# Optimization experiments

Hardware: AMD Instinct MI355X
Metric: run time of the kernel (lower is better)

## Reference

```python
import jax, jax.numpy as jnp
import numpy as np

B, C, G, E, R, T, L, K = 8, 192, 256, 384, 4, 8192, 3, 3
DILATIONS = (1, 3, 9)
EPS = 1e-5


def setup_inputs() -> dict:
    key = jax.random.key(0)
    ks = jax.random.split(key, 16)
    s = 0.05
    return {
        'x': jax.random.normal(ks[0], (B, C, T), jnp.float32),
        'x_mask': jnp.ones((B, 1, T), jnp.float32),
        'g': jax.random.normal(ks[1], (B, G, 1), jnp.float32),
        'dconv_w': jax.random.normal(ks[2], (L, C, K), jnp.float32) * s,
        'dconv_b': jax.random.normal(ks[3], (L, C), jnp.float32) * s,
        'ln_gamma': jnp.ones((L, C), jnp.float32),
        'ln_beta': jnp.zeros((L, C), jnp.float32),
        'p1_w': jax.random.normal(ks[4], (L, E, C), jnp.float32) * s,
        'p1_b': jax.random.normal(ks[5], (L, E), jnp.float32) * s,
        'p1_ain_w': jax.random.normal(ks[6], (L, C * R, G), jnp.float32) * 0.01,
        'p1_ain_b': jnp.zeros((L, C * R), jnp.float32),
        'p1_aout_w': jax.random.normal(ks[7], (L, E * R, G), jnp.float32) * 0.01,
        'p1_aout_b': jnp.zeros((L, E * R), jnp.float32),
        'p2_w': jax.random.normal(ks[8], (L, C, E), jnp.float32) * s,
        'p2_b': jax.random.normal(ks[9], (L, C), jnp.float32) * s,
        'p2_ain_w': jax.random.normal(ks[10], (L, E * R, G), jnp.float32) * 0.01,
        'p2_ain_b': jnp.zeros((L, E * R), jnp.float32),
        'p2_aout_w': jax.random.normal(ks[11], (L, C * R, G), jnp.float32) * 0.01,
        'p2_aout_b': jnp.zeros((L, C * R), jnp.float32),
    }


def _causal_dconv(x, w, b, dilation):
    # x: [B,C,T]; w: [C,K] depthwise kernel; matches flip/pad/conv/flip in torch module
    xf = jnp.flip(x, 2)
    xf = jnp.pad(xf, ((0, 0), (0, 0), (0, (K - 1) * dilation)))
    y = jax.lax.conv_general_dilated(
        xf, w[:, None, :], window_strides=(1,), padding='VALID',
        rhs_dilation=(dilation,), dimension_numbers=('NCH', 'OIH', 'NCH'),
        feature_group_count=C)
    y = y + b[None, :, None]
    return jnp.flip(y, 2)


def _layernorm_c(x, gamma, beta):
    # LayerNorm over channel axis (axis=1)
    mu = jnp.mean(x, axis=1, keepdims=True)
    var = jnp.mean(jnp.square(x - mu), axis=1, keepdims=True)
    xn = (x - mu) * jax.lax.rsqrt(var + EPS)
    return xn * gamma[None, :, None] + beta[None, :, None]


def _lora(x, g2, w_main, b_main, ain_w, ain_b, aout_w, aout_b, cin, cout):
    # main 1x1 conv
    x_ = jnp.einsum('oc,bcl->bol', w_main, x) + b_main[None, :, None]
    a_in = (g2 @ ain_w.T + ain_b).reshape(-1, cin, R)      # [B,cin,R]
    a_out = (g2 @ aout_w.T + aout_b).reshape(-1, R, cout)  # [B,R,cout]
    t = jnp.einsum('bcl,bcr->brl', x, a_in)
    low = jnp.einsum('brl,brc->bcl', t, a_out)
    return x_ + low


def reference(x, x_mask, g, dconv_w, dconv_b, ln_gamma, ln_beta,
              p1_w, p1_b, p1_ain_w, p1_ain_b, p1_aout_w, p1_aout_b,
              p2_w, p2_b, p2_ain_w, p2_ain_b, p2_aout_w, p2_aout_b):
    g2 = g[:, :, 0]  # [B,G]
    x = x * x_mask
    for i in range(L):
        residual = x
        h = _causal_dconv(x, dconv_w[i], dconv_b[i], DILATIONS[i])
        h = _layernorm_c(h, ln_gamma[i], ln_beta[i])
        h = h * x_mask
        h = _lora(h, g2, p1_w[i], p1_b[i], p1_ain_w[i], p1_ain_b[i],
                  p1_aout_w[i], p1_aout_b[i], C, E)
        h = jax.nn.gelu(h, approximate=False)
        h = _lora(h, g2, p2_w[i], p2_b[i], p2_ain_w[i], p2_ain_b[i],
                  p2_aout_w[i], p2_aout_b[i], E, C)
        x = residual + h
    return x
```

## Files before the change

kernel.cpp:

```cpp
#include <hip/hip_runtime.h>
#include <hip/hip_bf16.h>

#define B_ 8
#define C_ 192
#define G_ 256
#define E_ 384
#define R_ 4
#define T_ 8192
#define L_ 3
#define K_ 3

typedef __attribute__((ext_vector_type(4))) float f32x4;
typedef __attribute__((ext_vector_type(8))) short bf16x8;
typedef __attribute__((ext_vector_type(4))) short bf16x4;

static __device__ __forceinline__ float bf2f(short u) {
    union { float f; unsigned int i; } z;
    z.i = ((unsigned int)(unsigned short)u) << 16;
    return z.f;
}

static __device__ __forceinline__ float gelu_fast(float x) {
    float x2 = x * x;
    float inner = fmaf(0.044715f * x, x2, x);
    float e = __expf(1.5957691216057308f * inner);
    float r = 1.0f / (e + 1.0f);
    float t = fmaf(-2.0f, r, 1.0f);
    float s = 0.5f * x;
    return fmaf(s, t, s);
}

__global__ __launch_bounds__(256) void adapters_kernel(
    const float* __restrict__ g2,
    const float* __restrict__ w0, const float* __restrict__ bi0, float* __restrict__ o0,
    const float* __restrict__ w1, const float* __restrict__ bi1, float* __restrict__ o1,
    const float* __restrict__ w2, const float* __restrict__ bi2, float* __restrict__ o2,
    const float* __restrict__ w3, const float* __restrict__ bi3, float* __restrict__ o3)
{
    const int N0 = L_ * B_ * (C_ * R_);
    const int N1 = L_ * B_ * (E_ * R_);
    int idx = blockIdx.x * 256 + threadIdx.x;
    const float* w; const float* bi; float* o; int rows; int li;
    if (idx < N0)                      { w=w0; bi=bi0; o=o0; rows=C_*R_; li=idx; }
    else if ((idx -= N0) < N1)         { w=w1; bi=bi1; o=o1; rows=E_*R_; li=idx; }
    else if ((idx -= N1) < N1)         { w=w2; bi=bi2; o=o2; rows=E_*R_; li=idx; }
    else if ((idx -= N1) < N0)         { w=w3; bi=bi3; o=o3; rows=C_*R_; li=idx; }
    else return;
    int bb = li & 7;
    int lr = li >> 3;
    const float4* wr = (const float4*)(w + (size_t)lr * G_);
    const float4* gb = (const float4*)(g2 + (size_t)bb * G_);
    float s = bi[lr];
#pragma unroll 8
    for (int g = 0; g < G_ / 4; ++g) {
        float4 a = gb[g], b = wr[g];
        s = fmaf(a.x, b.x, s); s = fmaf(a.y, b.y, s);
        s = fmaf(a.z, b.z, s); s = fmaf(a.w, b.w, s);
    }
    o[((size_t)(lr / rows) * B_ + bb) * rows + (lr % rows)] = s;
}

__global__ __launch_bounds__(256) void builds_kernel(
    const float* __restrict__ p1w, const float* __restrict__ p2w,
    const float* __restrict__ A1in, const float* __restrict__ A1out,
    const float* __restrict__ A2in, const float* __restrict__ A2out,
    __hip_bfloat16* __restrict__ W1, __hip_bfloat16* __restrict__ W2)
{
    const int W1B = (L_ * B_ * E_ * C_) / 256;
    int blk = blockIdx.x;
    if (blk < W1B) {
        int idx = blk * 256 + threadIdx.x;
        int c = idx % C_;
        int e = (idx / C_) % E_;
        int b = (idx / (C_ * E_)) % B_;
        int l = idx / (C_ * E_ * B_);
        float v = p1w[((size_t)l * E_ + e) * C_ + c];
        const float* ai = A1in + ((size_t)l * B_ + b) * (C_ * R_);
        const float* ao = A1out + ((size_t)l * B_ + b) * (R_ * E_);
#pragma unroll
        for (int r = 0; r < R_; ++r) v = fmaf(ai[c * R_ + r], ao[r * E_ + e], v);
        W1[idx] = __float2bfloat16(v);
    } else {
        int idx = (blk - W1B) * 256 + threadIdx.x;
        int e = idx % E_;
        int c = (idx / E_) % C_;
        int b = (idx / (C_ * E_)) % B_;
        int l = idx / (C_ * E_ * B_);
        float v = p2w[((size_t)l * C_ + c) * E_ + e];
        const float* ai = A2in + ((size_t)l * B_ + b) * (E_ * R_);
        const float* ao = A2out + ((size_t)l * B_ + b) * (R_ * C_);
#pragma unroll
        for (int r = 0; r < R_; ++r) v = fmaf(ai[e * R_ + r], ao[r * C_ + c], v);
        W2[idx] = __float2bfloat16(v);
    }
}

__global__ __launch_bounds__(256) void transpose_in_kernel(
    const float* __restrict__ x, const float* __restrict__ mask,
    __hip_bfloat16* __restrict__ xw)
{
    __shared__ float tile[64][65];
    int b = blockIdx.z, c0 = blockIdx.y * 64, t0 = blockIdx.x * 64;
#pragma unroll
    for (int it = 0; it < 4; ++it) {
        int i = it * 256 + threadIdx.x;
        int r = i >> 4, cq = i & 15;
        float4 xv = *(const float4*)(&x[((size_t)b * C_ + c0 + r) * T_ + t0 + cq * 4]);
        float4 mv = *(const float4*)(&mask[(size_t)b * T_ + t0 + cq * 4]);
        tile[r][cq * 4 + 0] = xv.x * mv.x;
        tile[r][cq * 4 + 1] = xv.y * mv.y;
        tile[r][cq * 4 + 2] = xv.z * mv.z;
        tile[r][cq * 4 + 3] = xv.w * mv.w;
    }
    __syncthreads();
#pragma unroll
    for (int it = 0; it < 4; ++it) {
        int i = it * 256 + threadIdx.x;
        int r = i >> 4, cq = i & 15;
        union { __hip_bfloat16 h[4]; int2 i2; } u;
#pragma unroll
        for (int j = 0; j < 4; ++j) u.h[j] = __float2bfloat16(tile[cq * 4 + j][r]);
        *(int2*)(&xw[((size_t)b * T_ + t0 + r) * C_ + c0 + cq * 4]) = u.i2;
    }
}

__global__ __launch_bounds__(256, 2) void ffn_fused_kernel(
    const __hip_bfloat16* __restrict__ xin, __hip_bfloat16* __restrict__ xout,
    const float* __restrict__ dw, const float* __restrict__ db,
    const float* __restrict__ gamma, const float* __restrict__ beta,
    const float* __restrict__ mask,
    const __hip_bfloat16* __restrict__ W1, const float* __restrict__ b1,
    const __hip_bfloat16* __restrict__ W2, const float* __restrict__ b2,
    int dil, float* __restrict__ outF)
{
    __shared__ __align__(16) char smem[75776];
    __hip_bfloat16 (*Hs)[C_ + 8]  = (__hip_bfloat16 (*)[C_ + 8])smem;
    __hip_bfloat16 (*H1s)[E_ + 8] = (__hip_bfloat16 (*)[E_ + 8])(smem + 25600);
    float (*Tile)[68] = (float (*)[68])smem;

    const int bid = blockIdx.x;
    const int b = bid & 7;
    const int t0 = (bid >> 3) * 64;
    const int tid = threadIdx.x;
    const int wv = tid >> 6, lane = tid & 63;
    const int llo = lane & 15, lhi = lane >> 4;
    const size_t xbase = (size_t)b * T_ * C_;

    {
        const int grp = tid >> 4, gl = tid & 15;
        const int cbase = gl * 12;
        float4 wf[9], dbf[3], gaf[3], bef[3];
#pragma unroll
        for (int q = 0; q < 9; ++q) wf[q] = *(const float4*)(dw + cbase * 3 + q * 4);
#pragma unroll
        for (int q = 0; q < 3; ++q) {
            dbf[q] = *(const float4*)(db + cbase + q * 4);
            gaf[q] = *(const float4*)(gamma + cbase + q * 4);
            bef[q] = *(const float4*)(beta + cbase + q * 4);
        }
#pragma unroll
        for (int rr = 0; rr < 4; ++rr) {
            int tl = grp * 4 + rr;
            int t = t0 + tl;
            float v[12];
#pragma unroll
            for (int j = 0; j < 12; ++j) v[j] = ((const float*)dbf)[j];
#pragma unroll
            for (int k3 = 0; k3 < 3; ++k3) {
                int tt = t - k3 * dil;
                if (tt >= 0) {
                    const __hip_bfloat16* rp = xin + xbase + (size_t)tt * C_ + cbase;
#pragma unroll
                    for (int q = 0; q < 3; ++q) {
                        bf16x4 xv = *(const bf16x4*)(rp + q * 4);
#pragma unroll
                        for (int jj = 0; jj < 4; ++jj) {
                            int j = q * 4 + jj;
                            v[j] = fmaf(((const float*)wf)[j * 3 + k3], bf2f(xv[jj]), v[j]);
                        }
                    }
                }
            }
            float s = 0.f, sq = 0.f;
#pragma unroll
            for (int j = 0; j < 12; ++j) { s += v[j]; sq = fmaf(v[j], v[j], sq); }
#pragma unroll
            for (int o = 1; o <= 8; o <<= 1) {
                s += __shfl_xor(s, o, 64);
                sq += __shfl_xor(sq, o, 64);
            }
            float mu = s * (1.f / C_);
            float var = fmaf(sq, 1.f / C_, -mu * mu);
            float rs = rsqrtf(var + 1e-5f);
            float m = mask[(size_t)b * T_ + t];
            union { __hip_bfloat16 h[12]; int2 i2[3]; } u;
#pragma unroll
            for (int j = 0; j < 12; ++j) {
                float xn = (v[j] - mu) * rs;
                u.h[j] = __float2bfloat16(
                    fmaf(xn, ((const float*)gaf)[j], ((const float*)bef)[j]) * m);
            }
#pragma unroll
            for (int q = 0; q < 3; ++q)
                *(int2*)(&Hs[tl][cbase + q * 4]) = u.i2[q];
        }
    }
    __syncthreads();

    const __hip_bfloat16* w1p = W1 + (size_t)b * E_ * C_
        + (size_t)(wv * 96 + llo) * C_ + lhi * 8;
    f32x4 acc1[6][4] = {};
    {
        bf16x8 af[3][6], bfr[2][4];
#pragma unroll
        for (int mf = 0; mf < 6; ++mf) {
            af[0][mf] = *(const bf16x8*)(w1p + (size_t)mf * 16 * C_);
            af[1][mf] = *(const bf16x8*)(w1p + (size_t)mf * 16 * C_ + 32);
        }
#pragma unroll
        for (int nf = 0; nf < 4; ++nf)
            bfr[0][nf] = *(const bf16x8*)(&Hs[nf * 16 + llo][lhi * 8]);
#pragma unroll
        for (int kc = 0; kc < 6; ++kc) {
            const int cur = kc % 3;
            const int pf  = (kc + 2) % 3;
            const int bc  = kc & 1;
            if (kc < 4) {
#pragma unroll
                for (int mf = 0; mf < 6; ++mf)
                    af[pf][mf] = *(const bf16x8*)(w1p + (size_t)mf * 16 * C_ + (kc + 2) * 32);
            }
            if (kc < 5) {
#pragma unroll
                for (int nf = 0; nf < 4; ++nf)
                    bfr[bc ^ 1][nf] = *(const bf16x8*)(&Hs[nf * 16 + llo][(kc + 1) * 32 + lhi * 8]);
            }
#pragma unroll
            for (int mf = 0; mf < 6; ++mf)
#pragma unroll
                for (int nf = 0; nf < 4; ++nf)
                    acc1[mf][nf] = __builtin_amdgcn_mfma_f32_16x16x32_bf16(
                        af[cur][mf], bfr[bc][nf], acc1[mf][nf], 0, 0, 0);
        }
    }

#pragma unroll
    for (int mf = 0; mf < 6; ++mf) {
        int e0 = wv * 96 + mf * 16 + lhi * 4;
        float4 b1v = *(const float4*)(b1 + e0);
#pragma unroll
        for (int nf = 0; nf < 4; ++nf) {
            union { __hip_bfloat16 h[4]; int2 i2; } u;
#pragma unroll
            for (int j = 0; j < 4; ++j) {
                float xx = acc1[mf][nf][j] + ((const float*)&b1v)[j];
                u.h[j] = __float2bfloat16(gelu_fast(xx));
            }
            *(int2*)(&H1s[nf * 16 + llo][e0]) = u.i2;
        }
    }
    __syncthreads();

    const __hip_bfloat16* w2p = W2 + (size_t)b * C_ * E_
        + (size_t)(wv * 48 + llo) * E_ + lhi * 8;
    f32x4 acc2[3][4] = {};
    {
        bf16x8 af[3][3], bfr[2][4];
#pragma unroll
        for (int mf = 0; mf < 3; ++mf) {
            af[0][mf] = *(const bf16x8*)(w2p + (size_t)mf * 16 * E_);
            af[1][mf] = *(const bf16x8*)(w2p + (size_t)mf * 16 * E_ + 32);
        }
#pragma unroll
        for (int nf = 0; nf < 4; ++nf)
            bfr[0][nf] = *(const bf16x8*)(&H1s[nf * 16 + llo][lhi * 8]);
#pragma unroll
        for (int kc = 0; kc < 12; ++kc) {
            const int cur = kc % 3;
            const int pf  = (kc + 2) % 3;
            const int bc  = kc & 1;
            if (kc < 10) {
#pragma unroll
                for (int mf = 0; mf < 3; ++mf)
                    af[pf][mf] = *(const bf16x8*)(w2p + (size_t)mf * 16 * E_ + (kc + 2) * 32);
            }
            if (kc < 11) {
#pragma unroll
                for (int nf = 0; nf < 4; ++nf)
                    bfr[bc ^ 1][nf] = *(const bf16x8*)(&H1s[nf * 16 + llo][(kc + 1) * 32 + lhi * 8]);
            }
#pragma unroll
            for (int mf = 0; mf < 3; ++mf)
#pragma unroll
                for (int nf = 0; nf < 4; ++nf)
                    acc2[mf][nf] = __builtin_amdgcn_mfma_f32_16x16x32_bf16(
                        af[cur][mf], bfr[bc][nf], acc2[mf][nf], 0, 0, 0);
        }
    }

    if (outF == nullptr) {
#pragma unroll
        for (int mf = 0; mf < 3; ++mf) {
            int c0 = wv * 48 + mf * 16 + lhi * 4;
            float4 b2v = *(const float4*)(b2 + c0);
#pragma unroll
            for (int nf = 0; nf < 4; ++nf) {
                int t = t0 + nf * 16 + llo;
                const __hip_bfloat16* pr = xin + xbase + (size_t)t * C_ + c0;
                __hip_bfloat16* po = xout + xbase + (size_t)t * C_ + c0;
                union { __hip_bfloat16 h[4]; int2 i2; } ui, uo;
                ui.i2 = *(const int2*)pr;
#pragma unroll
                for (int j = 0; j < 4; ++j)
                    uo.h[j] = __float2bfloat16(
                        bf2f(*(short*)&ui.h[j]) + acc2[mf][nf][j] + ((const float*)&b2v)[j]);
                *(int2*)po = uo.i2;
            }
        }
    } else {
        __syncthreads();
#pragma unroll
        for (int mf = 0; mf < 3; ++mf) {
            int c0 = wv * 48 + mf * 16 + lhi * 4;
            float4 b2v = *(const float4*)(b2 + c0);
#pragma unroll
            for (int nf = 0; nf < 4; ++nf) {
                int tl = nf * 16 + llo;
                const __hip_bfloat16* pr = xin + xbase + (size_t)(t0 + tl) * C_ + c0;
                union { __hip_bfloat16 h[4]; int2 i2; } ui;
                ui.i2 = *(const int2*)pr;
#pragma unroll
                for (int j = 0; j < 4; ++j)
                    Tile[c0 + j][tl] =
                        bf2f(*(short*)&ui.h[j]) + acc2[mf][nf][j] + ((const float*)&b2v)[j];
            }
        }
        __syncthreads();
#pragma unroll
        for (int it = 0; it < 12; ++it) {
            int i = it * 256 + tid;
            int r = i >> 4, tq = i & 15;
            float4 o = *(const float4*)(&Tile[r][tq * 4]);
            *(float4*)(&outF[((size_t)b * C_ + r) * T_ + t0 + tq * 4]) = o;
        }
    }
}

extern "C" void kernel_launch(void* const* d_in, const int* in_sizes, int n_in,
                              void* d_out, int out_size, void* d_ws, size_t ws_size,
                              hipStream_t stream) {
    const float* x        = (const float*)d_in[0];
    const float* x_mask   = (const float*)d_in[1];
    const float* g        = (const float*)d_in[2];
    const float* dconv_w  = (const float*)d_in[3];
    const float* dconv_b  = (const float*)d_in[4];
    const float* ln_gamma = (const float*)d_in[5];
    const float* ln_beta  = (const float*)d_in[6];
    const float* p1_w     = (const float*)d_in[7];
    const float* p1_b     = (const float*)d_in[8];
    const float* p1_ain_w = (const float*)d_in[9];
    const float* p1_ain_b = (const float*)d_in[10];
    const float* p1_aout_w= (const float*)d_in[11];
    const float* p1_aout_b= (const float*)d_in[12];
    const float* p2_w     = (const float*)d_in[13];
    const float* p2_b     = (const float*)d_in[14];
    const float* p2_ain_w = (const float*)d_in[15];
    const float* p2_ain_b = (const float*)d_in[16];
    const float* p2_aout_w= (const float*)d_in[17];
    const float* p2_aout_b= (const float*)d_in[18];

    char* ws = (char*)d_ws;
    size_t off = 0;
    __hip_bfloat16* xwA = (__hip_bfloat16*)(ws + off); off += (size_t)B_ * T_ * C_ * 2;
    __hip_bfloat16* xwB = (__hip_bfloat16*)(ws + off); off += (size_t)B_ * T_ * C_ * 2;
    __hip_bfloat16* W1 = (__hip_bfloat16*)(ws + off);  off += (size_t)L_ * B_ * E_ * C_ * 2;
    __hip_bfloat16* W2 = (__hip_bfloat16*)(ws + off);  off += (size_t)L_ * B_ * C_ * E_ * 2;
    float* A1in  = (float*)(ws + off); off += (size_t)L_ * B_ * C_ * R_ * 4;
    float* A1out = (float*)(ws + off); off += (size_t)L_ * B_ * R_ * E_ * 4;
    float* A2in  = (float*)(ws + off); off += (size_t)L_ * B_ * E_ * R_ * 4;
    float* A2out = (float*)(ws + off); off += (size_t)L_ * B_ * R_ * C_ * 4;

    {
        int total = L_ * B_ * (2 * C_ * R_ + 2 * E_ * R_);
        adapters_kernel<<<(total + 255) / 256, 256, 0, stream>>>(
            g,
            p1_ain_w, p1_ain_b, A1in,
            p1_aout_w, p1_aout_b, A1out,
            p2_ain_w, p2_ain_b, A2in,
            p2_aout_w, p2_aout_b, A2out);
    }
    {
        int w1blocks = (L_ * B_ * E_ * C_) / 256;
        builds_kernel<<<2 * w1blocks, 256, 0, stream>>>(
            p1_w, p2_w, A1in, A1out, A2in, A2out, W1, W2);
    }

    transpose_in_kernel<<<dim3(T_ / 64, C_ / 64, B_), 256, 0, stream>>>(x, x_mask, xwA);

    const int DILS[3] = {1, 3, 9};
    __hip_bfloat16* bufs[2] = {xwA, xwB};
    for (int l = 0; l < L_; ++l) {
        float* outF = (l == L_ - 1) ? (float*)d_out : nullptr;
        ffn_fused_kernel<<<(T_ / 64) * B_, 256, 0, stream>>>(
            bufs[l & 1], bufs[(l & 1) ^ 1],
            dconv_w + l * C_ * K_, dconv_b + l * C_,
            ln_gamma + l * C_, ln_beta + l * C_, x_mask,
            W1 + (size_t)l * B_ * E_ * C_, p1_b + l * E_,
            W2 + (size_t)l * B_ * C_ * E_, p2_b + l * C_, DILS[l], outF);
    }
}
```

Before: 231.8 us.

## Give each wave its own 16-token slice and drop block-wide barriers

Work is now split by token instead of by output channel: each wave takes 16 tokens and computes all 384 hidden and 192 output channels for them, keeping its activations in a private shared-memory slice. This removes the two __syncthreads between the conv/layernorm, first GEMM and second GEMM stages. In exchange, every wave reads the full W1 and W2 from global or L2 memory with no register double-buffering, which is 4x more weight traffic per block. It also holds 24 accumulator fragments per lane, which raises register pressure.

```diff
diff --git a/kernel.cpp b/kernel.cpp
--- a/kernel.cpp
+++ b/kernel.cpp
@@ -134,20 +134,22 @@
     int dil, float* __restrict__ outF)
 {
     __shared__ __align__(16) char smem[75776];
-    __hip_bfloat16 (*Hs)[C_ + 8]  = (__hip_bfloat16 (*)[C_ + 8])smem;
-    __hip_bfloat16 (*H1s)[E_ + 8] = (__hip_bfloat16 (*)[E_ + 8])(smem + 25600);
-    float (*Tile)[68] = (float (*)[68])smem;
-
     const int bid = blockIdx.x;
     const int b = bid & 7;
     const int t0 = (bid >> 3) * 64;
     const int tid = threadIdx.x;
     const int wv = tid >> 6, lane = tid & 63;
     const int llo = lane & 15, lhi = lane >> 4;
+    const int t0w = t0 + wv * 16;
     const size_t xbase = (size_t)b * T_ * C_;
 
+    __hip_bfloat16 (*Hw)[C_ + 8] =
+        (__hip_bfloat16 (*)[C_ + 8])(smem + (size_t)wv * 16 * (C_ + 8) * 2);
+    __hip_bfloat16 (*H1w)[E_ + 8] =
+        (__hip_bfloat16 (*)[E_ + 8])(smem + 25600 + (size_t)wv * 16 * (E_ + 8) * 2);
+
     {
-        const int grp = tid >> 4, gl = tid & 15;
+        const int grp = lane >> 4, gl = lane & 15;
         const int cbase = gl * 12;
         float4 wf[9], dbf[3], gaf[3], bef[3];
 #pragma unroll
@@ -161,7 +163,7 @@
 #pragma unroll
         for (int rr = 0; rr < 4; ++rr) {
             int tl = grp * 4 + rr;
-            int t = t0 + tl;
+            int t = t0w + tl;
             float v[12];
 #pragma unroll
             for (int j = 0; j < 12; ++j) v[j] = ((const float*)dbf)[j];
@@ -202,137 +204,79 @@
             }
 #pragma unroll
             for (int q = 0; q < 3; ++q)
-                *(int2*)(&Hs[tl][cbase + q * 4]) = u.i2[q];
-        }
-    }
-    __syncthreads();
-
-    const __hip_bfloat16* w1p = W1 + (size_t)b * E_ * C_
-        + (size_t)(wv * 96 + llo) * C_ + lhi * 8;
-    f32x4 acc1[6][4] = {};
-    {
-        bf16x8 af[3][6], bfr[2][4];
-#pragma unroll
-        for (int mf = 0; mf < 6; ++mf) {
-            af[0][mf] = *(const bf16x8*)(w1p + (size_t)mf * 16 * C_);
-            af[1][mf] = *(const bf16x8*)(w1p + (size_t)mf * 16 * C_ + 32);
-        }
-#pragma unroll
-        for (int nf = 0; nf < 4; ++nf)
-            bfr[0][nf] = *(const bf16x8*)(&Hs[nf * 16 + llo][lhi * 8]);
-#pragma unroll
-        for (int kc = 0; kc < 6; ++kc) {
-            const int cur = kc % 3;
-            const int pf  = (kc + 2) % 3;
-            const int bc  = kc & 1;
-            if (kc < 4) {
-#pragma unroll
-                for (int mf = 0; mf < 6; ++mf)
-                    af[pf][mf] = *(const bf16x8*)(w1p + (size_t)mf * 16 * C_ + (kc + 2) * 32);
-            }
-            if (kc < 5) {
-#pragma unroll
-                for (int nf = 0; nf < 4; ++nf)
-                    bfr[bc ^ 1][nf] = *(const bf16x8*)(&Hs[nf * 16 + llo][(kc + 1) * 32 + lhi * 8]);
-            }
-#pragma unroll
-            for (int mf = 0; mf < 6; ++mf)
-#pragma unroll
-                for (int nf = 0; nf < 4; ++nf)
-                    acc1[mf][nf] = __builtin_amdgcn_mfma_f32_16x16x32_bf16(
-                        af[cur][mf], bfr[bc][nf], acc1[mf][nf], 0, 0, 0);
-        }
-    }
-
-#pragma unroll
-    for (int mf = 0; mf < 6; ++mf) {
-        int e0 = wv * 96 + mf * 16 + lhi * 4;
+                *(int2*)(&Hw[tl][cbase + q * 4]) = u.i2[q];
+        }
+    }
+
+    const __hip_bfloat16* w1p = W1 + (size_t)b * E_ * C_ + (size_t)llo * C_ + lhi * 8;
+    f32x4 acc1[24] = {};
+#pragma unroll
+    for (int kc = 0; kc < 6; ++kc) {
+        bf16x8 bfr = *(const bf16x8*)(&Hw[llo][kc * 32 + lhi * 8]);
+#pragma unroll
+        for (int mf = 0; mf < 24; ++mf) {
+            bf16x8 af = *(const bf16x8*)(w1p + (size_t)mf * 16 * C_ + kc * 32);
+            acc1[mf] = __builtin_amdgcn_mfma_f32_16x16x32_bf16(af, bfr, acc1[mf], 0, 0, 0);
+        }
+    }
+
+#pragma unroll
+    for (int mf = 0; mf < 24; ++mf) {
+        int e0 = mf * 16 + lhi * 4;
         float4 b1v = *(const float4*)(b1 + e0);
-#pragma unroll
-        for (int nf = 0; nf < 4; ++nf) {
-            union { __hip_bfloat16 h[4]; int2 i2; } u;
-#pragma unroll
-            for (int j = 0; j < 4; ++j) {
-                float xx = acc1[mf][nf][j] + ((const float*)&b1v)[j];
-                u.h[j] = __float2bfloat16(gelu_fast(xx));
-            }
-            *(int2*)(&H1s[nf * 16 + llo][e0]) = u.i2;
-        }
-    }
-    __syncthreads();
-
-    const __hip_bfloat16* w2p = W2 + (size_t)b * C_ * E_
-        + (size_t)(wv * 48 + llo) * E_ + lhi * 8;
-    f32x4 acc2[3][4] = {};
-    {
-        bf16x8 af[3][3], bfr[2][4];
-#pragma unroll
-        for (int mf = 0; mf < 3; ++mf) {
-            af[0][mf] = *(const bf16x8*)(w2p + (size_t)mf * 16 * E_);
-            af[1][mf] = *(const bf16x8*)(w2p + (size_t)mf * 16 * E_ + 32);
-        }
-#pragma unroll
-        for (int nf = 0; nf < 4; ++nf)
-            bfr[0][nf] = *(const bf16x8*)(&H1s[nf * 16 + llo][lhi * 8]);
-#pragma unroll
-        for (int kc = 0; kc < 12; ++kc) {
-            const int cur = kc % 3;
-            const int pf  = (kc + 2) % 3;
-            const int bc  = kc & 1;
-            if (kc < 10) {
-#pragma unroll
-                for (int mf = 0; mf < 3; ++mf)
-                    af[pf][mf] = *(const bf16x8*)(w2p + (size_t)mf * 16 * E_ + (kc + 2) * 32);
-            }
-            if (kc < 11) {
-#pragma unroll
-                for (int nf = 0; nf < 4; ++nf)
-                    bfr[bc ^ 1][nf] = *(const bf16x8*)(&H1s[nf * 16 + llo][(kc + 1) * 32 + lhi * 8]);
-            }
-#pragma unroll
-            for (int mf = 0; mf < 3; ++mf)
-#pragma unroll
-                for (int nf = 0; nf < 4; ++nf)
-                    acc2[mf][nf] = __builtin_amdgcn_mfma_f32_16x16x32_bf16(
-                        af[cur][mf], bfr[bc][nf], acc2[mf][nf], 0, 0, 0);
+        union { __hip_bfloat16 h[4]; int2 i2; } u;
+#pragma unroll
+        for (int j = 0; j < 4; ++j) {
+            float xx = acc1[mf][j] + ((const float*)&b1v)[j];
+            u.h[j] = __float2bfloat16(gelu_fast(xx));
+        }
+        *(int2*)(&H1w[llo][e0]) = u.i2;
+    }
+
+    const __hip_bfloat16* w2p = W2 + (size_t)b * C_ * E_ + (size_t)llo * E_ + lhi * 8;
+    f32x4 acc2[12] = {};
+#pragma unroll
+    for (int kc = 0; kc < 12; ++kc) {
+        bf16x8 bfr = *(const bf16x8*)(&H1w[llo][kc * 32 + lhi * 8]);
+#pragma unroll
+        for (int mf = 0; mf < 12; ++mf) {
+            bf16x8 af = *(const bf16x8*)(w2p + (size_t)mf * 16 * E_ + kc * 32);
+            acc2[mf] = __builtin_amdgcn_mfma_f32_16x16x32_bf16(af, bfr, acc2[mf], 0, 0, 0);
         }
     }
 
     if (outF == nullptr) {
-#pragma unroll
-        for (int mf = 0; mf < 3; ++mf) {
-            int c0 = wv * 48 + mf * 16 + lhi * 4;
+        int t = t0w + llo;
+        const __hip_bfloat16* pr = xin + xbase + (size_t)t * C_;
+        __hip_bfloat16* po = xout + xbase + (size_t)t * C_;
+#pragma unroll
+        for (int mf = 0; mf < 12; ++mf) {
+            int c0 = mf * 16 + lhi * 4;
             float4 b2v = *(const float4*)(b2 + c0);
-#pragma unroll
-            for (int nf = 0; nf < 4; ++nf) {
-                int t = t0 + nf * 16 + llo;
-                const __hip_bfloat16* pr = xin + xbase + (size_t)t * C_ + c0;
-                __hip_bfloat16* po = xout + xbase + (size_t)t * C_ + c0;
-                union { __hip_bfloat16 h[4]; int2 i2; } ui, uo;
-                ui.i2 = *(const int2*)pr;
-#pragma unroll
-                for (int j = 0; j < 4; ++j)
-                    uo.h[j] = __float2bfloat16(
-                        bf2f(*(short*)&ui.h[j]) + acc2[mf][nf][j] + ((const float*)&b2v)[j]);
-                *(int2*)po = uo.i2;
-            }
+            union { __hip_bfloat16 h[4]; int2 i2; } ui, uo;
+            ui.i2 = *(const int2*)(pr + c0);
+#pragma unroll
+            for (int j = 0; j < 4; ++j)
+                uo.h[j] = __float2bfloat16(
+                    bf2f(*(short*)&ui.h[j]) + acc2[mf][j] + ((const float*)&b2v)[j]);
+            *(int2*)(po + c0) = uo.i2;
         }
     } else {
+        float (*Tile)[68] = (float (*)[68])smem;
         __syncthreads();
-#pragma unroll
-        for (int mf = 0; mf < 3; ++mf) {
-            int c0 = wv * 48 + mf * 16 + lhi * 4;
-            float4 b2v = *(const float4*)(b2 + c0);
-#pragma unroll
-            for (int nf = 0; nf < 4; ++nf) {
-                int tl = nf * 16 + llo;
-                const __hip_bfloat16* pr = xin + xbase + (size_t)(t0 + tl) * C_ + c0;
+        {
+            int tl = wv * 16 + llo;
+            const __hip_bfloat16* pr = xin + xbase + (size_t)(t0 + tl) * C_;
+#pragma unroll
+            for (int mf = 0; mf < 12; ++mf) {
+                int c0 = mf * 16 + lhi * 4;
+                float4 b2v = *(const float4*)(b2 + c0);
                 union { __hip_bfloat16 h[4]; int2 i2; } ui;
-                ui.i2 = *(const int2*)pr;
+                ui.i2 = *(const int2*)(pr + c0);
 #pragma unroll
                 for (int j = 0; j < 4; ++j)
                     Tile[c0 + j][tl] =
-                        bf2f(*(short*)&ui.h[j]) + acc2[mf][nf][j] + ((const float*)&b2v)[j];
+                        bf2f(*(short*)&ui.h[j]) + acc2[mf][j] + ((const float*)&b2v)[j];
             }
         }
         __syncthreads();
```

Measured after the change: 505.2 us. 2.18x slower.
